# Performance work log

Hardware: AMD Instinct MI355X
Metric: run time of the kernel (lower is better)

Reference implementation:

```python
import jax, jax.numpy as jnp
import numpy as np

TEMPERATURE = 1.0
PRED_PER_IM = 100
INVALID = np.arange(60, 80)  # invalid class logit indices (constant)


def setup_inputs() -> dict:
    key = jax.random.key(0)
    k1, k2, k3, k4, k5 = jax.random.split(key, 5)
    B, Q, C = 256, 1000, 81
    return {
        "pred_logits": jax.random.normal(k1, (B, Q, C), jnp.float32),
        "pred_obj": jax.random.normal(k2, (B, Q), jnp.float32),
        "pred_boxes": jax.random.uniform(k3, (B, Q, 4), jnp.float32),  # cxcywh in [0,1)
        "pred_unk": jax.random.normal(k4, (B, Q), jnp.float32),
        "target_sizes": jax.random.uniform(k5, (B, 2), jnp.float32, minval=480.0, maxval=1333.0),  # (h, w)
    }


def _postprocess(pred_logits, pred_obj, pred_boxes, pred_unk, target_sizes):
    B, Q, C = pred_logits.shape
    # mask invalid classes with a huge negative logit
    logits = pred_logits.at[:, :, INVALID].set(-1e11)
    obj_prob = jnp.exp(-TEMPERATURE * pred_obj)[..., None]            # [B,Q,1]
    prob = obj_prob * jax.nn.sigmoid(logits)                          # [B,Q,C]
    prob = prob.at[:, :, INVALID].set(0.0)
    unk = jax.nn.sigmoid(pred_unk)                                    # [B,Q]
    prob = prob * (1.0 - unk[..., None])
    prob = prob.at[:, :, -1].set(obj_prob[..., 0] * unk)              # unknown class slot
    # flattened top-k over (query, class)
    scores, idx = jax.lax.top_k(prob.reshape(B, Q * C), PRED_PER_IM)  # [B,K]
    topk_boxes = idx // C
    labels = idx % C
    # cxcywh -> xyxy
    cx, cy, w, h = jnp.split(pred_boxes, 4, axis=-1)
    xyxy = jnp.concatenate([cx - 0.5 * w, cy - 0.5 * h, cx + 0.5 * w, cy + 0.5 * h], axis=-1)
    boxes = jnp.take_along_axis(xyxy, topk_boxes[..., None], axis=1)  # [B,K,4]
    img_h, img_w = target_sizes[:, 0], target_sizes[:, 1]
    scale = jnp.stack([img_w, img_h, img_w, img_h], axis=1)           # [B,4]
    boxes = boxes * scale[:, None, :]
    return scores, labels, boxes


def reference(pred_logits, pred_obj, pred_boxes, pred_unk, target_sizes):
    return _postprocess(pred_logits, pred_obj, pred_boxes, pred_unk, target_sizes)
```

## Files before the change

### kernel.cpp

```cpp
#include <hip/hip_runtime.h>
#include <math.h>

#define BATCH  256
#define NQ     1000
#define NC     81
#define QC     81000
#define CHUNKS (QC / 4)
#define TOPK   100
#define NBINS  4096
#define CAP    2048
#define NT     1024

__device__ __forceinline__ float sigmoidf(float x) {
    if (x >= 0.f) return 1.f / (1.f + expf(-x));
    float e = expf(x);
    return e / (1.f + e);
}

__device__ __forceinline__ float fast_sig(float x) {
    return __builtin_amdgcn_rcpf(1.f + __expf(-x));
}

struct Smem {
    float    P[NQ];
    float    Pm2[NQ];
    float    op[NQ];
    float    omun[NQ];
    float    last[NQ];
    unsigned hist[NBINS];
    uint2    cand[CAP];
    int      rowlist[NQ];
    unsigned nrows;
    unsigned cnt;
    unsigned thr;
};

__device__ unsigned scan_threshold(Smem& s, int tid) {
    __syncthreads();
    if (tid < 64) {
        unsigned c = 0;
        #pragma unroll
        for (int j = 0; j < 64; j += 4) {
            uint4 h = *(const uint4*)&s.hist[tid * 64 + j];
            c += h.x + h.y + h.z + h.w;
        }
        unsigned ssum = c;
        #pragma unroll
        for (int off = 1; off < 64; off <<= 1) {
            unsigned o = __shfl_down(ssum, off, 64);
            if (tid + off < 64) ssum += o;
        }
        unsigned long long bal = __ballot(ssum >= TOPK);
        int cb = 63 - __clzll(bal);
        unsigned tb = 0;
        if (cb >= 0) {
            unsigned S_cb = __shfl(ssum, cb, 64);
            unsigned c_cb = __shfl(c, cb, 64);
            unsigned acc  = S_cb - c_cb;
            unsigned fs = s.hist[cb * 64 + tid];
            #pragma unroll
            for (int off = 1; off < 64; off <<= 1) {
                unsigned o = __shfl_down(fs, off, 64);
                if (tid + off < 64) fs += o;
            }
            unsigned long long bal2 = __ballot(acc + fs >= TOPK);
            int fb = 63 - __clzll(bal2);
            tb = (unsigned)(cb * 64 + fb);
        }
        if (tid == 0) s.thr = tb;
    }
    __syncthreads();
    return s.thr;
}

template <bool COLLECT>
__device__ __forceinline__ void proc_chunk(Smem& s, const float4& v4, int q, int c,
                                           unsigned thbits) {
    float xs[4] = {v4.x, v4.y, v4.z, v4.w};
    #pragma unroll
    for (int k = 0; k < 4; ++k) {
        int ck = c + k, qk = q;
        if (ck >= NC) { ck -= NC; ++qk; }
        if (ck < 60) {
            unsigned u = __float_as_uint(s.P[qk] * fast_sig(xs[k]));
            if (u >= thbits) {
                if (!COLLECT) {
                    atomicAdd(&s.hist[u >> 19], 1u);
                } else {
                    float pv = (s.op[qk] * sigmoidf(xs[k])) * s.omun[qk];
                    unsigned p = atomicAdd(&s.cnt, 1u);
                    if (p < CAP)
                        s.cand[p] = make_uint2(__float_as_uint(pv),
                                               (unsigned)(qk * NC + ck));
                }
            }
        }
    }
}

__device__ void build_rows(Smem& s, unsigned thbits, int tid) {
    __syncthreads();
    if (tid == 0) s.nrows = 0;
    __syncthreads();
    for (int q = tid; q < NQ; q += NT)
        if (__float_as_uint(s.Pm2[q]) >= thbits)
            s.rowlist[atomicAdd(&s.nrows, 1u)] = q;
    __syncthreads();
}

template <bool COLLECT>
__device__ void scan_rows(Smem& s, const float4* __restrict__ lg4,
                          unsigned thbits, int tid) {
    const int total = (int)s.nrows * 21;
    for (int idx = tid; idx < total; idx += NT) {
        int r  = idx / 21;
        int j  = idx - r * 21;
        int q  = s.rowlist[r];
        int e0 = NC * q;
        int i4 = ((e0 + 3) >> 2) + j;
        if (4 * i4 < e0 + NC) {
            float4 v4 = lg4[i4];
            proc_chunk<COLLECT>(s, v4, q, 4 * i4 - e0, thbits);
        }
    }
}

__device__ void collect80(Smem& s, unsigned thbits, int tid) {
    for (int q = tid; q < NQ; q += NT) {
        unsigned u = __float_as_uint(s.last[q]);
        if (u >= thbits) {
            unsigned p = atomicAdd(&s.cnt, 1u);
            if (p < CAP) s.cand[p] = make_uint2(u, (unsigned)(q * NC + 80));
        }
    }
}

__global__ __launch_bounds__(NT) void postprocess_kernel(
    const float* __restrict__ logits,
    const float* __restrict__ obj,
    const float* __restrict__ boxes,
    const float* __restrict__ unk,
    const float* __restrict__ tsz,
    float* __restrict__ out)
{
    __shared__ Smem s;
    const int b   = blockIdx.x;
    const int tid = threadIdx.x;
    const float4* lg4 = (const float4*)(logits + (size_t)b * QC);

    *(uint4*)&s.hist[tid * 4] = make_uint4(0u, 0u, 0u, 0u);
    if (tid == 0) s.cnt = 0;
    for (int q = tid; q < NQ; q += NT) {
        float op = expf(-obj[b * NQ + q]);
        float un = sigmoidf(unk[b * NQ + q]);
        float om = 1.f - un;
        s.op[q] = op; s.omun[q] = om; s.P[q] = op * om; s.last[q] = op * un;
    }
    __syncthreads();

    for (int q = tid; q < NQ; q += NT) {
        float pm = s.P[q];
        if (q + 1 < NQ) pm = fmaxf(pm, s.P[q + 1]);
        s.Pm2[q] = pm;
        atomicAdd(&s.hist[__float_as_uint(s.last[q]) >> 19], 1u);
    }

    unsigned t0 = scan_threshold(s, tid);

    build_rows(s, t0 << 19, tid);
    scan_rows<false>(s, lg4, t0 << 19, tid);

    unsigned tF = scan_threshold(s, tid);

    unsigned thC = ((tF >= 1) ? tF - 1 : 0) << 19;
    build_rows(s, thC, tid);
    scan_rows<true>(s, lg4, thC, tid);
    collect80(s, thC, tid);
    __syncthreads();

    if (s.cnt > CAP) {
        __syncthreads();
        if (tid == 0) s.cnt = 0;
        __syncthreads();
        scan_rows<true>(s, lg4, tF << 19, tid);
        collect80(s, tF << 19, tid);
        __syncthreads();
    }

    const int m = (int)min(s.cnt, (unsigned)CAP);

    const float* bx = boxes + (size_t)b * NQ * 4;
    const float img_h = tsz[b * 2 + 0];
    const float img_w = tsz[b * 2 + 1];
    float* o_sc = out + (size_t)b * TOPK;
    float* o_lb = out + (size_t)BATCH * TOPK + (size_t)b * TOPK;
    float* o_bx = out + (size_t)2 * BATCH * TOPK + (size_t)b * TOPK * 4;

    for (int i = tid; i < m; i += NT) {
        uint2 ci = s.cand[i];
        int r = 0;
        for (int j = 0; j < m; ++j) {
            uint2 cj = s.cand[j];
            r += (cj.x > ci.x) || (cj.x == ci.x && cj.y < ci.y);
        }
        if (r < TOPK) {
            int ei = (int)ci.y;
            o_sc[r] = __uint_as_float(ci.x);
            o_lb[r] = (float)(ei % NC);
            int q = ei / NC;
            float cx = bx[q * 4 + 0];
            float cy = bx[q * 4 + 1];
            float w  = bx[q * 4 + 2];
            float h  = bx[q * 4 + 3];
            o_bx[r * 4 + 0] = (cx - 0.5f * w) * img_w;
            o_bx[r * 4 + 1] = (cy - 0.5f * h) * img_h;
            o_bx[r * 4 + 2] = (cx + 0.5f * w) * img_w;
            o_bx[r * 4 + 3] = (cy + 0.5f * h) * img_h;
        }
    }
}

extern "C" void kernel_launch(void* const* d_in, const int* in_sizes, int n_in,
                              void* d_out, int out_size, void* d_ws, size_t ws_size,
                              hipStream_t stream) {
    const float* pred_logits = (const float*)d_in[0];
    const float* pred_obj    = (const float*)d_in[1];
    const float* pred_boxes  = (const float*)d_in[2];
    const float* pred_unk    = (const float*)d_in[3];
    const float* target_sz   = (const float*)d_in[4];
    float* out = (float*)d_out;
    postprocess_kernel<<<BATCH, NT, 0, stream>>>(
        pred_logits, pred_obj, pred_boxes, pred_unk, target_sz, out);
}
```

Before: 136.8 us.

## Fuse histogram and candidate collection into one pass over logits

Merges the second histogram pass and the collection pass into one scan that both updates the histogram and stores approximate candidates in a larger shared buffer. The final threshold then filters those stored candidates and recomputes precise scores with a few gathered logit loads, instead of rescanning rows. A fallback rescan stays for buffer overflow. The histogram read order in the threshold scan is also rotated per lane to reduce LDS bank conflicts. The price is more shared memory (larger candidate arrays), which may lower occupancy, plus extra atomics in the fused pass.

Result: no change. 138.7 us (+1.4%).

```diff
diff --git a/kernel.cpp b/kernel.cpp
--- a/kernel.cpp
+++ b/kernel.cpp
@@ -5,10 +5,10 @@
 #define NQ     1000
 #define NC     81
 #define QC     81000
-#define CHUNKS (QC / 4)
 #define TOPK   100
 #define NBINS  4096
-#define CAP    2048
+#define CAP    6144
+#define CAP2   2048
 #define NT     1024
 
 __device__ __forceinline__ float sigmoidf(float x) {
@@ -29,9 +29,11 @@
     float    last[NQ];
     unsigned hist[NBINS];
     uint2    cand[CAP];
+    uint2    cand2[CAP2];
     int      rowlist[NQ];
     unsigned nrows;
     unsigned cnt;
+    unsigned cnt2;
     unsigned thr;
 };
 
@@ -39,9 +41,11 @@
     __syncthreads();
     if (tid < 64) {
         unsigned c = 0;
+        int rot = tid & 15;
         #pragma unroll
-        for (int j = 0; j < 64; j += 4) {
-            uint4 h = *(const uint4*)&s.hist[tid * 64 + j];
+        for (int j = 0; j < 16; ++j) {
+            int jj = ((j + rot) & 15) * 4;
+            uint4 h = *(const uint4*)&s.hist[tid * 64 + jj];
             c += h.x + h.y + h.z + h.w;
         }
         unsigned ssum = c;
@@ -73,31 +77,6 @@
     return s.thr;
 }
 
-template <bool COLLECT>
-__device__ __forceinline__ void proc_chunk(Smem& s, const float4& v4, int q, int c,
-                                           unsigned thbits) {
-    float xs[4] = {v4.x, v4.y, v4.z, v4.w};
-    #pragma unroll
-    for (int k = 0; k < 4; ++k) {
-        int ck = c + k, qk = q;
-        if (ck >= NC) { ck -= NC; ++qk; }
-        if (ck < 60) {
-            unsigned u = __float_as_uint(s.P[qk] * fast_sig(xs[k]));
-            if (u >= thbits) {
-                if (!COLLECT) {
-                    atomicAdd(&s.hist[u >> 19], 1u);
-                } else {
-                    float pv = (s.op[qk] * sigmoidf(xs[k])) * s.omun[qk];
-                    unsigned p = atomicAdd(&s.cnt, 1u);
-                    if (p < CAP)
-                        s.cand[p] = make_uint2(__float_as_uint(pv),
-                                               (unsigned)(qk * NC + ck));
-                }
-            }
-        }
-    }
-}
-
 __device__ void build_rows(Smem& s, unsigned thbits, int tid) {
     __syncthreads();
     if (tid == 0) s.nrows = 0;
@@ -108,9 +87,8 @@
     __syncthreads();
 }
 
-template <bool COLLECT>
-__device__ void scan_rows(Smem& s, const float4* __restrict__ lg4,
-                          unsigned thbits, int tid) {
+__device__ void scan_fused(Smem& s, const float4* __restrict__ lg4,
+                           unsigned thbits, int tid) {
     const int total = (int)s.nrows * 21;
     for (int idx = tid; idx < total; idx += NT) {
         int r  = idx / 21;
@@ -120,17 +98,74 @@
         int i4 = ((e0 + 3) >> 2) + j;
         if (4 * i4 < e0 + NC) {
             float4 v4 = lg4[i4];
-            proc_chunk<COLLECT>(s, v4, q, 4 * i4 - e0, thbits);
-        }
-    }
-}
-
-__device__ void collect80(Smem& s, unsigned thbits, int tid) {
+            int c = 4 * i4 - e0;
+            float xs[4] = {v4.x, v4.y, v4.z, v4.w};
+            #pragma unroll
+            for (int k = 0; k < 4; ++k) {
+                int ck = c + k, qk = q;
+                if (ck >= NC) { ck -= NC; ++qk; }
+                if (ck < 60) {
+                    unsigned u = __float_as_uint(s.P[qk] * fast_sig(xs[k]));
+                    if (u >= thbits) {
+                        atomicAdd(&s.hist[u >> 19], 1u);
+                        unsigned p = atomicAdd(&s.cnt, 1u);
+                        if (p < CAP)
+                            s.cand[p] = make_uint2(u, (unsigned)(qk * NC + ck));
+                    }
+                }
+            }
+        }
+    }
+}
+
+__device__ void collect_precise(Smem& s, const float4* __restrict__ lg4,
+                                unsigned thbits, int tid) {
+    const int total = (int)s.nrows * 21;
+    for (int idx = tid; idx < total; idx += NT) {
+        int r  = idx / 21;
+        int j  = idx - r * 21;
+        int q  = s.rowlist[r];
+        int e0 = NC * q;
+        int i4 = ((e0 + 3) >> 2) + j;
+        if (4 * i4 < e0 + NC) {
+            float4 v4 = lg4[i4];
+            int c = 4 * i4 - e0;
+            float xs[4] = {v4.x, v4.y, v4.z, v4.w};
+            #pragma unroll
+            for (int k = 0; k < 4; ++k) {
+                int ck = c + k, qk = q;
+                if (ck >= NC) { ck -= NC; ++qk; }
+                if (ck < 60) {
+                    unsigned u = __float_as_uint(s.P[qk] * fast_sig(xs[k]));
+                    if (u >= thbits) {
+                        float pv = (s.op[qk] * sigmoidf(xs[k])) * s.omun[qk];
+                        unsigned p = atomicAdd(&s.cnt2, 1u);
+                        if (p < CAP2)
+                            s.cand2[p] = make_uint2(__float_as_uint(pv),
+                                                    (unsigned)(qk * NC + ck));
+                    }
+                }
+            }
+        }
+    }
+}
+
+__device__ void collect80_approx(Smem& s, unsigned thbits, int tid) {
     for (int q = tid; q < NQ; q += NT) {
         unsigned u = __float_as_uint(s.last[q]);
         if (u >= thbits) {
             unsigned p = atomicAdd(&s.cnt, 1u);
             if (p < CAP) s.cand[p] = make_uint2(u, (unsigned)(q * NC + 80));
+        }
+    }
+}
+
+__device__ void collect80_precise(Smem& s, unsigned thbits, int tid) {
+    for (int q = tid; q < NQ; q += NT) {
+        unsigned u = __float_as_uint(s.last[q]);
+        if (u >= thbits) {
+            unsigned p = atomicAdd(&s.cnt2, 1u);
+            if (p < CAP2) s.cand2[p] = make_uint2(u, (unsigned)(q * NC + 80));
         }
     }
 }
@@ -146,10 +181,11 @@
     __shared__ Smem s;
     const int b   = blockIdx.x;
     const int tid = threadIdx.x;
-    const float4* lg4 = (const float4*)(logits + (size_t)b * QC);
+    const float*  lgf = logits + (size_t)b * QC;
+    const float4* lg4 = (const float4*)lgf;
 
     *(uint4*)&s.hist[tid * 4] = make_uint4(0u, 0u, 0u, 0u);
-    if (tid == 0) s.cnt = 0;
+    if (tid == 0) { s.cnt = 0; s.cnt2 = 0; }
     for (int q = tid; q < NQ; q += NT) {
         float op = expf(-obj[b * NQ + q]);
         float un = sigmoidf(unk[b * NQ + q]);
@@ -165,29 +201,52 @@
         atomicAdd(&s.hist[__float_as_uint(s.last[q]) >> 19], 1u);
     }
 
-    unsigned t0 = scan_threshold(s, tid);
-
-    build_rows(s, t0 << 19, tid);
-    scan_rows<false>(s, lg4, t0 << 19, tid);
-
-    unsigned tF = scan_threshold(s, tid);
-
+    unsigned t0  = scan_threshold(s, tid);
+    unsigned thA = ((t0 >= 1) ? t0 - 1 : 0) << 19;
+
+    build_rows(s, thA, tid);
+    scan_fused(s, lg4, thA, tid);
+    collect80_approx(s, thA, tid);
+    __syncthreads();
+
+    unsigned tF  = scan_threshold(s, tid);
     unsigned thC = ((tF >= 1) ? tF - 1 : 0) << 19;
-    build_rows(s, thC, tid);
-    scan_rows<true>(s, lg4, thC, tid);
-    collect80(s, thC, tid);
-    __syncthreads();
-
-    if (s.cnt > CAP) {
-        __syncthreads();
-        if (tid == 0) s.cnt = 0;
-        __syncthreads();
-        scan_rows<true>(s, lg4, tF << 19, tid);
-        collect80(s, tF << 19, tid);
-        __syncthreads();
-    }
-
-    const int m = (int)min(s.cnt, (unsigned)CAP);
+
+    unsigned total = s.cnt;
+    if (total <= CAP) {
+        for (int i = tid; i < (int)total; i += NT) {
+            uint2 cd = s.cand[i];
+            if (cd.x >= thC) {
+                unsigned q = cd.y / NC;
+                unsigned c = cd.y - q * NC;
+                float pv;
+                if (c == 80) pv = s.last[q];
+                else         pv = (s.op[q] * sigmoidf(lgf[cd.y])) * s.omun[q];
+                unsigned p = atomicAdd(&s.cnt2, 1u);
+                if (p < CAP2) s.cand2[p] = make_uint2(__float_as_uint(pv), cd.y);
+            }
+        }
+        __syncthreads();
+    }
+    if (total > CAP || s.cnt2 > CAP2) {
+        __syncthreads();
+        if (tid == 0) s.cnt2 = 0;
+        __syncthreads();
+        build_rows(s, thC, tid);
+        collect_precise(s, lg4, thC, tid);
+        collect80_precise(s, thC, tid);
+        __syncthreads();
+        if (s.cnt2 > CAP2) {
+            __syncthreads();
+            if (tid == 0) s.cnt2 = 0;
+            __syncthreads();
+            collect_precise(s, lg4, tF << 19, tid);
+            collect80_precise(s, tF << 19, tid);
+            __syncthreads();
+        }
+    }
+
+    const int m = (int)min(s.cnt2, (unsigned)CAP2);
 
     const float* bx = boxes + (size_t)b * NQ * 4;
     const float img_h = tsz[b * 2 + 0];
@@ -197,10 +256,10 @@
     float* o_bx = out + (size_t)2 * BATCH * TOPK + (size_t)b * TOPK * 4;
 
     for (int i = tid; i < m; i += NT) {
-        uint2 ci = s.cand[i];
+        uint2 ci = s.cand2[i];
         int r = 0;
         for (int j = 0; j < m; ++j) {
-            uint2 cj = s.cand[j];
+            uint2 cj = s.cand2[j];
             r += (cj.x > ci.x) || (cj.x == ci.x && cj.y < ci.y);
         }
         if (r < TOPK) {
```
